# Kernel tuning notes

Measured on AMD Instinct MI355X. Metric: run time of the kernel, lower is better.

## Reference

```python
import jax, jax.numpy as jnp
import numpy as np
from jax import lax

# Model dims (match init_kwargs config)
HID = 2048      # hidden_size
NH = 64         # num_heads
P = 64          # head_dim
N = 128         # ssm_state_size
G = 1           # n_groups
CS = 256        # chunk_size
K = 4           # conv kernel
D_INNER = NH * P                  # 4096
CONV_DIM = D_INNER + 2 * G * N    # 4352
PROJ = D_INNER + CONV_DIM + NH    # 8512
EPS = 1e-5
BATCH, SEQ = 2, 2048


def setup_inputs() -> dict:
    key = jax.random.key(0)
    ks = jax.random.split(key, 8)
    hidden_states = jax.random.normal(ks[0], (BATCH, SEQ, HID), dtype=jnp.float32)
    W_in = jax.random.normal(ks[1], (PROJ, HID), dtype=jnp.float32) * 0.02
    conv_w = jax.random.normal(ks[2], (CONV_DIM, 1, K), dtype=jnp.float32) * 0.2
    conv_b = jax.random.normal(ks[3], (CONV_DIM,), dtype=jnp.float32) * 0.02
    # dt_bias initialized like inv-softplus of dt in [1e-3, 1e-1]
    dt = jnp.exp(jax.random.uniform(ks[4], (NH,)) * (np.log(0.1) - np.log(0.001)) + np.log(0.001))
    dt_bias = (dt + jnp.log(-jnp.expm1(-dt))).astype(jnp.float32)
    A_log = jnp.log(jnp.arange(1, NH + 1, dtype=jnp.float32))
    D_param = jnp.ones((NH,), dtype=jnp.float32)
    norm_w = jnp.ones((D_INNER,), dtype=jnp.float32)
    W_out = jax.random.normal(ks[5], (HID, D_INNER), dtype=jnp.float32) * 0.02
    return {"hidden_states": hidden_states, "W_in": W_in, "conv_w": conv_w,
            "conv_b": conv_b, "dt_bias": dt_bias, "A_log": A_log,
            "D_param": D_param, "norm_w": norm_w, "W_out": W_out}


def _segsum(x):
    # x: (..., c) -> (..., c, c); seg[i, j] = sum_{j < k <= i} x_k (diag 0), -inf above diag
    T = x.shape[-1]
    xc = jnp.cumsum(x, axis=-1)
    seg = xc[..., :, None] - xc[..., None, :]
    mask = jnp.tril(jnp.ones((T, T), dtype=bool))
    return jnp.where(mask, seg, -jnp.inf)


def _mamba2_forward(hidden_states, W_in, conv_w, conv_b, dt_bias, A_log, D_param, norm_w, W_out):
    B_, L_ = hidden_states.shape[:2]
    proj = hidden_states @ W_in.T                           # (b, l, PROJ)
    z = proj[..., :D_INNER]                                 # gate
    xBC = proj[..., D_INNER:D_INNER + CONV_DIM]
    dt = proj[..., D_INNER + CONV_DIM:]                     # (b, l, NH)

    # depthwise causal conv1d + silu
    xc = lax.conv_general_dilated(
        jnp.transpose(xBC, (0, 2, 1)), conv_w,
        window_strides=(1,), padding=[(K - 1, 0)],
        feature_group_count=CONV_DIM)                        # (b, CONV_DIM, l)
    xc = xc + conv_b[None, :, None]
    xBC = jax.nn.silu(jnp.transpose(xc, (0, 2, 1)))          # (b, l, CONV_DIM)

    x = xBC[..., :D_INNER].reshape(B_, L_, NH, P)
    Bm = xBC[..., D_INNER:D_INNER + G * N].reshape(B_, L_, G, N)
    Cm = xBC[..., D_INNER + G * N:].reshape(B_, L_, G, N)

    dt = jax.nn.softplus(dt + dt_bias)                       # (b, l, NH)
    A = -jnp.exp(A_log)                                      # (NH,)

    Bh = jnp.repeat(Bm, NH // G, axis=2)                     # (b, l, h, n)
    Ch = jnp.repeat(Cm, NH // G, axis=2)

    # ---- chunked SSD scan ----
    nc = L_ // CS
    x_dt = (x * dt[..., None]).reshape(B_, nc, CS, NH, P)    # (b, c, s, h, p)
    B_c = Bh.reshape(B_, nc, CS, NH, N)
    C_c = Ch.reshape(B_, nc, CS, NH, N)
    dA = jnp.transpose((dt * A).reshape(B_, nc, CS, NH), (0, 3, 1, 2))  # (b, h, c, s)
    A_cum = jnp.cumsum(dA, axis=-1)                          # (b, h, c, s)

    Lmat = jnp.exp(_segsum(dA))                              # (b, h, c, s, s)
    Y_diag = jnp.einsum('bclhn,bcshn,bhcls,bcshp->bclhp', C_c, B_c, Lmat, x_dt)

    decay_states = jnp.exp(A_cum[..., -1:] - A_cum)          # (b, h, c, s)
    states = jnp.einsum('bclhn,bhcl,bclhp->bchpn', B_c, decay_states, x_dt)

    da_last = A_cum[..., -1]                                 # (b, h, c)

    def step(prev, inp):
        s_k, d_k = inp                                       # (b,h,p,n), (b,h)
        new = prev * jnp.exp(d_k)[..., None, None] + s_k
        return new, prev

    _, prev_states = lax.scan(step, jnp.zeros((B_, NH, P, N), dtype=x.dtype),
                              (jnp.transpose(states, (1, 0, 2, 3, 4)),
                               jnp.transpose(da_last, (2, 0, 1))))
    prev_states = jnp.transpose(prev_states, (1, 2, 0, 3, 4))  # (b, h, c, p, n)

    Y_off = jnp.einsum('bclhn,bhcpn,bhcl->bclhp', C_c, prev_states, jnp.exp(A_cum))

    y = (Y_diag + Y_off).reshape(B_, L_, NH, P) + D_param[None, None, :, None] * x
    y = y.reshape(B_, L_, D_INNER)

    # gated grouped RMSNorm (norm_before_gate=False): norm(y * silu(z)) * w
    g = y * jax.nn.silu(z)
    gs = D_INNER // G
    gr = g.reshape(B_, L_, G, gs)
    var = jnp.mean(gr * gr, axis=-1, keepdims=True)
    gn = (gr * lax.rsqrt(var + EPS)).reshape(B_, L_, D_INNER) * norm_w

    return gn @ W_out.T                                      # (b, l, HID)


def reference(hidden_states, W_in, conv_w, conv_b, dt_bias, A_log, D_param, norm_w, W_out):
    return _mamba2_forward(hidden_states, W_in, conv_w, conv_b, dt_bias, A_log, D_param, norm_w, W_out)
```

## Files before the change

### kernel.cpp

```cpp
#include <hip/hip_runtime.h>

#define SEQLEN 2048
#define NHEADS 64
#define PDIM 64
#define NSTATE 128
#define CSIZE 256
#define NCHUNK 8
#define DINNER 4096
#define CONVD 4352
#define PROJD 8512

using s8v = __attribute__((ext_vector_type(8))) short;
using f4v = __attribute__((ext_vector_type(4))) float;
using bf8v = __attribute__((ext_vector_type(8))) __bf16;

__device__ __forceinline__ short f2bf(float x) {
  union { float f; unsigned u; } t; t.f = x;
  unsigned r = t.u + 0x7FFFu + ((t.u >> 16) & 1u);
  return (short)(r >> 16);
}
__device__ __forceinline__ float bf2f(short s) {
  union { unsigned u; float f; } t;
  t.u = ((unsigned)(unsigned short)s) << 16;
  return t.f;
}

__device__ __forceinline__ f4v mfma_bf16(s8v a, s8v b, f4v c) {
  return __builtin_amdgcn_mfma_f32_16x16x32_bf16(
      __builtin_bit_cast(bf8v, a), __builtin_bit_cast(bf8v, b), c, 0, 0, 0);
}

__device__ __forceinline__ void gll16(const void* g, void* l) {
  __builtin_amdgcn_global_load_lds(
      (const __attribute__((address_space(1))) unsigned*)g,
      (__attribute__((address_space(3))) unsigned*)l, 16, 0, 0);
}

__global__ __launch_bounds__(256) void cast_bf16_kernel(
    const float* __restrict__ in, short* __restrict__ out, int n4) {
  int i = blockIdx.x * 256 + threadIdx.x;
  if (i < n4) {
    float4 v = ((const float4*)in)[i];
    short4 o;
    o.x = f2bf(v.x); o.y = f2bf(v.y); o.z = f2bf(v.z); o.w = f2bf(v.w);
    ((short4*)out)[i] = o;
  }
}


#define G1_STAGE_A(dst, h, kt) do {                                          \
    _Pragma("unroll")                                                        \
    for (int it_ = 0; it_ < 2; ++it_) {                                      \
      int ci_ = it_ * 512 + tid;                                             \
      int r_ = ci_ >> 3;                                                     \
      int g_ = ((ci_ & 7) ^ (r_ & 7)) << 3;                                  \
      gll16(&A[(size_t)(tm0 + (h) * 128 + r_) * 2048 + (kt) * 64 + g_],      \
            &(dst)[(h) * 8192 + ci_ * 8]);                                   \
    }                                                                        \
  } while (0)

#define G1_STAGE_B(dst, h, kt) do {                                          \
    _Pragma("unroll")                                                        \
    for (int it_ = 0; it_ < 2; ++it_) {                                      \
      int ci_ = it_ * 512 + tid;                                             \
      int r_ = ci_ >> 3;                                                     \
      int g_ = ((ci_ & 7) ^ (r_ & 7)) << 3;                                  \
      int br_ = tn0 + (h) * 128 + r_;                                        \
      if (br_ > 8511) br_ = 8511;       \
      gll16(&B[(size_t)br_ * 2048 + (kt) * 64 + g_],                         \
            &(dst)[(h) * 8192 + ci_ * 8]);                                   \
    }                                                                        \
  } while (0)

#define RD_A(m, ks) \
  (*(const s8v*)&Ad[(wm + (m) * 16 + lr) * 64 + (((ks) * 4 + q) ^ sw7) * 8])
#define RD_B(n, ks) \
  (*(const s8v*)&Bd[(wn + (n) * 16 + lr) * 64 + (((ks) * 4 + q) ^ sw7) * 8])

#define G1_MFMA2(m0, x00, x01, x10, x11) do {                                \
    __builtin_amdgcn_s_setprio(1);                                           \
    _Pragma("unroll") for (int n = 0; n < 4; ++n)                            \
      acc[m0][n] = mfma_bf16(x00, bk0[n], acc[m0][n]);                       \
    _Pragma("unroll") for (int n = 0; n < 4; ++n)                            \
      acc[(m0) + 1][n] = mfma_bf16(x10, bk0[n], acc[(m0) + 1][n]);           \
    _Pragma("unroll") for (int n = 0; n < 4; ++n)                            \
      acc[m0][n] = mfma_bf16(x01, bk1[n], acc[m0][n]);                       \
    _Pragma("unroll") for (int n = 0; n < 4; ++n)                            \
      acc[(m0) + 1][n] = mfma_bf16(x11, bk1[n], acc[(m0) + 1][n]);           \
    __builtin_amdgcn_s_setprio(0);                                           \
  } while (0)

__global__ __launch_bounds__(512, 2) void gemm1_256(
    const short* __restrict__ A, const short* __restrict__ B,
    short* __restrict__ z, short* __restrict__ xbc, float* __restrict__ dtb,
    const float* __restrict__ dt_bias) {
  const int NT = 32;
  const int bid = blockIdx.x;
  const int sid = (bid & 7) * 68 + (bid >> 3);
  const int panel = sid / 136, rem = sid % 136;
  const int bx = rem >> 2, by = panel * 4 + (rem & 3);
  const int tm0 = by * 256, tn0 = bx * 256;
  __shared__ alignas(16) short lds[65536];
  const int tid = threadIdx.x;
  const int lane = tid & 63, wid = tid >> 6;
  const int wm = (wid >> 2) * 128, wn = (wid & 3) * 64;
  const int lr = lane & 15, q = lane >> 4;
  const int sw7 = lr & 7;

  f4v acc[8][4];
#pragma unroll
  for (int m = 0; m < 8; ++m)
#pragma unroll
    for (int n = 0; n < 4; ++n)
#pragma unroll
      for (int r = 0; r < 4; ++r) acc[m][n][r] = 0.f;

  {
    short* A0 = lds;
    short* B0 = lds + 16384;
    short* B1 = lds + 49152;
    G1_STAGE_A(A0, 0, 0); G1_STAGE_A(A0, 1, 0);
    G1_STAGE_B(B0, 0, 0); G1_STAGE_B(B0, 1, 0);
    G1_STAGE_B(B1, 0, 1); G1_STAGE_B(B1, 1, 1);
    asm volatile("s_waitcnt vmcnt(4)" ::: "memory");
    __builtin_amdgcn_s_barrier();
  }

  for (int t = 0; t < NT; ++t) {
    short* Ad = lds + ((t & 1) << 15);
    short* Bd = Ad + 16384;
    short* An = lds + (((t + 1) & 1) << 15);
    s8v bk0[4], bk1[4];
    {
#pragma unroll
      for (int n = 0; n < 4; ++n) { bk0[n] = RD_B(n, 0); bk1[n] = RD_B(n, 1); }
      s8v a00 = RD_A(0, 0), a01 = RD_A(0, 1);
      s8v a10 = RD_A(1, 0), a11 = RD_A(1, 1);
      if (t + 1 < NT) G1_STAGE_A(An, 0, t + 1);
      __builtin_amdgcn_s_barrier();
      G1_MFMA2(0, a00, a01, a10, a11);
      __builtin_amdgcn_s_barrier();
    }
    {
      s8v a00 = RD_A(2, 0), a01 = RD_A(2, 1);
      s8v a10 = RD_A(3, 0), a11 = RD_A(3, 1);
      if (t + 1 < NT) G1_STAGE_A(An, 1, t + 1);
      __builtin_amdgcn_s_barrier();
      G1_MFMA2(2, a00, a01, a10, a11);
      __builtin_amdgcn_s_barrier();
    }
    {
      s8v a00 = RD_A(4, 0), a01 = RD_A(4, 1);
      s8v a10 = RD_A(5, 0), a11 = RD_A(5, 1);
      if (t + 2 < NT) G1_STAGE_B(Bd, 0, t + 2);
      __builtin_amdgcn_s_barrier();
      G1_MFMA2(4, a00, a01, a10, a11);
      __builtin_amdgcn_s_barrier();
    }
    {
      s8v a00 = RD_A(6, 0), a01 = RD_A(6, 1);
      s8v a10 = RD_A(7, 0), a11 = RD_A(7, 1);
      if (t + 2 < NT) G1_STAGE_B(Bd, 1, t + 2);
      if (t < NT - 2) {
        asm volatile("s_waitcnt vmcnt(4)" ::: "memory");
      } else {
        asm volatile("s_waitcnt vmcnt(0)" ::: "memory");
      }
      __builtin_amdgcn_s_barrier();
      G1_MFMA2(6, a00, a01, a10, a11);
      __builtin_amdgcn_s_barrier();
    }
  }

  if (bx == 33) {
    if (wn == 0) {
#pragma unroll
      for (int m = 0; m < 8; ++m)
#pragma unroll
        for (int n = 0; n < 4; ++n) {
          int col = n * 16 + lr;
          float bias = dt_bias[col];
#pragma unroll
          for (int r = 0; r < 4; ++r) {
            int row = tm0 + wm + m * 16 + q * 4 + r;
            float v = acc[m][n][r] + bias;
            float sp = (v > 20.f) ? v : log1pf(expf(v));
            dtb[(size_t)row * NHEADS + col] = sp;
          }
        }
    }
    return;
  }
  short* outp; int stride, colbase;
  if (bx < 16) { outp = z;   stride = DINNER; colbase = tn0; }
  else         { outp = xbc; stride = CONVD;  colbase = tn0 - DINNER; }
  short* Cs = lds;
  for (int h = 0; h < 2; ++h) {
    __syncthreads();
    if ((wid >> 2) == h) {
#pragma unroll
      for (int m = 0; m < 8; ++m)
#pragma unroll
        for (int n = 0; n < 4; ++n)
#pragma unroll
          for (int r = 0; r < 4; ++r)
            Cs[(m * 16 + q * 4 + r) * 264 + wn + n * 16 + lr] =
                f2bf(acc[m][n][r]);
    }
    __syncthreads();
#pragma unroll
    for (int itr = 0; itr < 8; ++itr) {
      int idx = itr * 512 + tid;
      int r = idx >> 5, c8 = (idx & 31) * 8;
      s8v v = *(const s8v*)&Cs[r * 264 + c8];
      *(s8v*)&outp[(size_t)(tm0 + h * 128 + r) * stride + colbase + c8] = v;
    }
  }
}


#define G2_STAGE_A(dst, h, kt) do {                                          \
    _Pragma("unroll")                                                        \
    for (int it_ = 0; it_ < 2; ++it_) {                                      \
      int ci_ = it_ * 512 + tid;                                             \
      int r_ = ci_ >> 3;                                                     \
      int g_ = ((ci_ & 7) ^ (r_ & 7)) << 3;                                  \
      gll16(&Ag[(size_t)(tm0 + (h) * 128 + r_) * 4096 + (kt) * 64 + g_],     \
            &(dst)[(h) * 8192 + ci_ * 8]);                                   \
    }                                                                        \
  } while (0)

#define G2_STAGE_B(dst, h, kt) do {                                          \
    int ci_ = tid;                                                           \
    int r_ = ci_ >> 3;                                                       \
    int g_ = ((ci_ & 7) ^ (r_ & 7)) << 3;                                    \
    gll16(&Bg[(size_t)(tn0 + (h) * 64 + r_) * 4096 + (kt) * 64 + g_],        \
          &(dst)[(h) * 4096 + ci_ * 8]);                                     \
  } while (0)

#define RD_A2(m, ks) \
  (*(const s8v*)&Ad[(wm + (m) * 16 + lr) * 64 + (((ks) * 4 + q) ^ sw7) * 8])
#define RD_B2(n, ks) \
  (*(const s8v*)&Bd[(wn + (n) * 16 + lr) * 64 + (((ks) * 4 + q) ^ sw7) * 8])

#define G2_MFMA2(m0, x00, x01, x10, x11) do {                                \
    __builtin_amdgcn_s_setprio(1);                                           \
    _Pragma("unroll") for (int n = 0; n < 2; ++n)                            \
      acc[m0][n] = mfma_bf16(x00, bk0[n], acc[m0][n]);                       \
    _Pragma("unroll") for (int n = 0; n < 2; ++n)                            \
      acc[(m0) + 1][n] = mfma_bf16(x10, bk0[n], acc[(m0) + 1][n]);           \
    _Pragma("unroll") for (int n = 0; n < 2; ++n)                            \
      acc[m0][n] = mfma_bf16(x01, bk1[n], acc[m0][n]);                       \
    _Pragma("unroll") for (int n = 0; n < 2; ++n)                            \
      acc[(m0) + 1][n] = mfma_bf16(x11, bk1[n], acc[(m0) + 1][n]);           \
    __builtin_amdgcn_s_setprio(0);                                           \
  } while (0)

__global__ __launch_bounds__(512, 2) void gemm2_256x128(
    const short* __restrict__ Ag, const short* __restrict__ Bg,
    float* __restrict__ C) {
  const int NT = 64;
  const int bid = blockIdx.x;
  const int sid = (bid & 7) * 32 + (bid >> 3);
  const int panel = sid >> 6, rem = sid & 63;
  const int bx = rem >> 2, by = panel * 4 + (rem & 3);
  const int tm0 = by * 256, tn0 = bx * 128;
  __shared__ alignas(16) short lds[49152];
  const int tid = threadIdx.x;
  const int lane = tid & 63, wid = tid >> 6;
  const int wm = (wid >> 2) * 128, wn = (wid & 3) * 32;
  const int lr = lane & 15, q = lane >> 4;
  const int sw7 = lr & 7;

  f4v acc[8][2];
#pragma unroll
  for (int m = 0; m < 8; ++m)
#pragma unroll
    for (int n = 0; n < 2; ++n)
#pragma unroll
      for (int r = 0; r < 4; ++r) acc[m][n][r] = 0.f;

  {
    short* A0 = lds;
    short* B0 = lds + 16384;
    short* B1 = lds + 40960;
    G2_STAGE_A(A0, 0, 0); G2_STAGE_A(A0, 1, 0);
    G2_STAGE_B(B0, 0, 0); G2_STAGE_B(B0, 1, 0);
    G2_STAGE_B(B1, 0, 1); G2_STAGE_B(B1, 1, 1);
    asm volatile("s_waitcnt vmcnt(2)" ::: "memory");
    __builtin_amdgcn_s_barrier();
  }

  for (int t = 0; t < NT; ++t) {
    short* Ad = lds + (t & 1) * 24576;
    short* Bd = Ad + 16384;
    short* An = lds + ((t + 1) & 1) * 24576;
    s8v bk0[2], bk1[2];
    {
#pragma unroll
      for (int n = 0; n < 2; ++n) { bk0[n] = RD_B2(n, 0); bk1[n] = RD_B2(n, 1); }
      s8v a00 = RD_A2(0, 0), a01 = RD_A2(0, 1);
      s8v a10 = RD_A2(1, 0), a11 = RD_A2(1, 1);
      if (t + 1 < NT) G2_STAGE_A(An, 0, t + 1);
      __builtin_amdgcn_s_barrier();
      G2_MFMA2(0, a00, a01, a10, a11);
      __builtin_amdgcn_s_barrier();
    }
    {
      s8v a00 = RD_A2(2, 0), a01 = RD_A2(2, 1);
      s8v a10 = RD_A2(3, 0), a11 = RD_A2(3, 1);
      if (t + 1 < NT) G2_STAGE_A(An, 1, t + 1);
      __builtin_amdgcn_s_barrier();
      G2_MFMA2(2, a00, a01, a10, a11);
      __builtin_amdgcn_s_barrier();
    }
    {
      s8v a00 = RD_A2(4, 0), a01 = RD_A2(4, 1);
      s8v a10 = RD_A2(5, 0), a11 = RD_A2(5, 1);
      if (t + 2 < NT) G2_STAGE_B(Bd, 0, t + 2);
      __builtin_amdgcn_s_barrier();
      G2_MFMA2(4, a00, a01, a10, a11);
      __builtin_amdgcn_s_barrier();
    }
    {
      s8v a00 = RD_A2(6, 0), a01 = RD_A2(6, 1);
      s8v a10 = RD_A2(7, 0), a11 = RD_A2(7, 1);
      if (t + 2 < NT) G2_STAGE_B(Bd, 1, t + 2);
      if (t < NT - 2) {
        asm volatile("s_waitcnt vmcnt(2)" ::: "memory");
      } else {
        asm volatile("s_waitcnt vmcnt(0)" ::: "memory");
      }
      __builtin_amdgcn_s_barrier();
      G2_MFMA2(6, a00, a01, a10, a11);
      __builtin_amdgcn_s_barrier();
    }
  }

#pragma unroll
  for (int m = 0; m < 8; ++m)
#pragma unroll
    for (int n = 0; n < 2; ++n) {
      int r0 = tm0 + wm + m * 16 + q * 4;
      int c0 = tn0 + wn + n * 16 + lr;
#pragma unroll
      for (int r = 0; r < 4; ++r)
        C[(size_t)(r0 + r) * 2048 + c0] = acc[m][n][r];
    }
}

__global__ __launch_bounds__(256) void conv_silu_kernel(
    const short* __restrict__ xbc, const float* __restrict__ conv_w,
    const float* __restrict__ conv_b, short* __restrict__ xBCc) {
  int cc = blockIdx.x * 256 + threadIdx.x;
  int bl = blockIdx.y;
  int b = bl >> 11, l = bl & 2047;
  float4 wv = *(const float4*)&conv_w[cc * 4];
  float wk[4] = {wv.x, wv.y, wv.z, wv.w};
  float acc = conv_b[cc];
  const short* pbase = xbc + (size_t)(b * SEQLEN) * CONVD + cc;
#pragma unroll
  for (int k = 0; k < 4; k++) {
    int ls = l - 3 + k;
    if (ls >= 0) acc += bf2f(pbase[(size_t)ls * CONVD]) * wk[k];
  }
  float sv = acc / (1.f + expf(-acc));
  xBCc[(size_t)bl * CONVD + cc] = f2bf(sv);
}

__global__ __launch_bounds__(256) void ssd_states_kernel(
    const short* __restrict__ xBCc, const float* __restrict__ dtp,
    const float* __restrict__ A_log, short* __restrict__ states,
    float* __restrict__ da_last) {
  const int blk = blockIdx.x;
  const int h = blk & 63, cc = (blk >> 6) & 7, b = blk >> 9;
  const int tid = threadIdx.x;
  __shared__ float dt_s[CSIZE], Acum[CSIZE], w_s[CSIZE];
  __shared__ float xw[64][64];
  __shared__ float Bt[64][NSTATE];
  const size_t row0 = (size_t)(b * SEQLEN + cc * CSIZE);
  dt_s[tid] = dtp[(row0 + tid) * NHEADS + h];
  __syncthreads();
  if (tid == 0) {
    float Aval = -expf(A_log[h]);
    float s = 0.f;
    for (int i = 0; i < CSIZE; i++) { s += dt_s[i]; Acum[i] = s * Aval; }
    da_last[(size_t)(b * NHEADS + h) * NCHUNK + cc] = Acum[CSIZE - 1];
  }
  __syncthreads();
  float total = Acum[CSIZE - 1];
  w_s[tid] = dt_s[tid] * expf(total - Acum[tid]);
  float acc[4][8];
  for (int a = 0; a < 4; a++) for (int j = 0; j < 8; j++) acc[a][j] = 0.f;
  const int pi = (tid & 15) * 4, ni = (tid >> 4) * 8;
  for (int lt = 0; lt < 4; lt++) {
    __syncthreads();
    for (int i = 0; i < 4; i++) {
      int idx = tid + i * 256;
      int r = idx >> 4, c4 = (idx & 15) << 2;
      short4 v = *(const short4*)&xBCc[(row0 + lt * 64 + r) * CONVD + h * PDIM + c4];
      float wl = w_s[lt * 64 + r];
      xw[r][c4 + 0] = bf2f(v.x) * wl;
      xw[r][c4 + 1] = bf2f(v.y) * wl;
      xw[r][c4 + 2] = bf2f(v.z) * wl;
      xw[r][c4 + 3] = bf2f(v.w) * wl;
    }
    for (int i = 0; i < 8; i++) {
      int idx = tid + i * 256;
      int r = idx >> 5, c4 = (idx & 31) << 2;
      short4 v = *(const short4*)&xBCc[(row0 + lt * 64 + r) * CONVD + DINNER + c4];
      Bt[r][c4 + 0] = bf2f(v.x);
      Bt[r][c4 + 1] = bf2f(v.y);
      Bt[r][c4 + 2] = bf2f(v.z);
      Bt[r][c4 + 3] = bf2f(v.w);
    }
    __syncthreads();
    for (int l = 0; l < 64; l++) {
      float4 xv = *(const float4*)&xw[l][pi];
      float4 b0 = *(const float4*)&Bt[l][ni];
      float4 b1 = *(const float4*)&Bt[l][ni + 4];
      float xa[4] = {xv.x, xv.y, xv.z, xv.w};
      float bb[8] = {b0.x, b0.y, b0.z, b0.w, b1.x, b1.y, b1.z, b1.w};
      for (int a = 0; a < 4; a++)
        for (int j = 0; j < 8; j++)
          acc[a][j] += xa[a] * bb[j];
    }
  }
  const size_t sbase = (((size_t)b * NCHUNK + cc) * NHEADS + h) * (PDIM * NSTATE);
  for (int a = 0; a < 4; a++) {
    short o[8];
    for (int j = 0; j < 8; j++) o[j] = f2bf(acc[a][j]);
    *(s8v*)&states[sbase + (size_t)(pi + a) * NSTATE + ni] = *(const s8v*)o;
  }
}

__global__ __launch_bounds__(256) void scan_kernel(
    short* __restrict__ states, const float* __restrict__ da_last) {
  const int bh = blockIdx.x >> 2, sl = blockIdx.x & 3;
  const int b = bh >> 6, h = bh & 63;
  const int tid = threadIdx.x;
  float prev[8];
  for (int i = 0; i < 8; i++) prev[i] = 0.f;
  for (int c = 0; c < NCHUNK; c++) {
    const size_t base = (((size_t)b * NCHUNK + c) * NHEADS + h) * (PDIM * NSTATE)
                      + sl * 2048;
    const float d = expf(da_last[(size_t)bh * NCHUNK + c]);
    for (int i = 0; i < 8; i++) {
      size_t e = base + tid + i * 256;
      float s = bf2f(states[e]);
      states[e] = f2bf(prev[i]);
      prev[i] = prev[i] * d + s;
    }
  }
}

__global__ __launch_bounds__(256) void ssd_y_kernel(
    const short* __restrict__ xBCc, const float* __restrict__ dtp,
    const float* __restrict__ A_log, const float* __restrict__ D_param,
    const short* __restrict__ prevs, short* __restrict__ y) {
  const int blk = blockIdx.x;
  const int h = blk & 63, cc = (blk >> 6) & 7, b = blk >> 9;
  const int tid = threadIdx.x;
  const int lane = tid & 63, w = tid >> 6;
  const int lr = lane & 15, q = lane >> 4;
  __shared__ float dt_s[CSIZE];
  __shared__ float Acum[CSIZE];
  __shared__ short C_s[64][136];
  __shared__ short BP_s[64][136];
  __shared__ short xdtT[64][72];
  __shared__ short Mt[64][72];
  const size_t row0 = (size_t)(b * SEQLEN + cc * CSIZE);
  dt_s[tid] = dtp[(row0 + tid) * NHEADS + h];
  __syncthreads();
  if (tid == 0) {
    float Aval = -expf(A_log[h]);
    float s = 0.f;
    for (int i = 0; i < CSIZE; i++) { s += dt_s[i]; Acum[i] = s * Aval; }
  }
  const float Dh = D_param[h];
  const size_t prevbase = (((size_t)b * NCHUNK + cc) * NHEADS + h) * (PDIM * NSTATE);
  const int wl0 = w * 16;

  for (int lt = 0; lt < 4; lt++) {
    __syncthreads();
    for (int i = 0; i < 4; i++) {
      int idx = tid + i * 256;
      int r = idx >> 4, c8 = (idx & 15) << 3;
      *(s8v*)&C_s[r][c8] =
          *(const s8v*)&xBCc[(row0 + lt * 64 + r) * CONVD + DINNER + NSTATE + c8];
      *(s8v*)&BP_s[r][c8] = *(const s8v*)&prevs[prevbase + (size_t)r * NSTATE + c8];
    }
    __syncthreads();
    f4v acc[4];
    for (int j = 0; j < 4; j++) for (int r = 0; r < 4; r++) acc[j][r] = 0.f;
    for (int ks = 0; ks < 4; ks++) {
      s8v a = *(const s8v*)&C_s[wl0 + lr][ks * 32 + q * 8];
      for (int j = 0; j < 4; j++) {
        s8v bb = *(const s8v*)&BP_s[j * 16 + lr][ks * 32 + q * 8];
        acc[j] = mfma_bf16(a, bb, acc[j]);
      }
    }
    for (int r = 0; r < 4; r++) {
      float e = __expf(Acum[lt * 64 + wl0 + q * 4 + r]);
      for (int j = 0; j < 4; j++) acc[j][r] *= e;
    }
    for (int st = 0; st <= lt; st++) {
      __syncthreads();
      for (int i = 0; i < 4; i++) {
        int idx = tid + i * 256;
        int r = idx >> 4, c8 = (idx & 15) << 3;
        *(s8v*)&BP_s[r][c8] =
            *(const s8v*)&xBCc[(row0 + st * 64 + r) * CONVD + DINNER + c8];
      }
      for (int i = 0; i < 4; i++) {
        int idx = tid + i * 256;
        int r = idx >> 4, c4 = (idx & 15) << 2;
        float dtv = dt_s[st * 64 + r];
        short4 v = *(const short4*)&xBCc[(row0 + st * 64 + r) * CONVD + h * PDIM + c4];
        xdtT[c4 + 0][r] = f2bf(bf2f(v.x) * dtv);
        xdtT[c4 + 1][r] = f2bf(bf2f(v.y) * dtv);
        xdtT[c4 + 2][r] = f2bf(bf2f(v.z) * dtv);
        xdtT[c4 + 3][r] = f2bf(bf2f(v.w) * dtv);
      }
      __syncthreads();
      f4v sacc[4];
      for (int j = 0; j < 4; j++) for (int r = 0; r < 4; r++) sacc[j][r] = 0.f;
      for (int ks = 0; ks < 4; ks++) {
        s8v a = *(const s8v*)&C_s[wl0 + lr][ks * 32 + q * 8];
        for (int j = 0; j < 4; j++) {
          s8v bb = *(const s8v*)&BP_s[j * 16 + lr][ks * 32 + q * 8];
          sacc[j] = mfma_bf16(a, bb, sacc[j]);
        }
      }
      int lbase = lt * 64 + wl0 + q * 4;
      for (int j = 0; j < 4; j++) {
        int sg = st * 64 + j * 16 + lr;
        for (int r = 0; r < 4; r++) {
          int ll = lbase + r;
          float m = (sg <= ll) ? sacc[j][r] * __expf(Acum[ll] - Acum[sg]) : 0.f;
          Mt[wl0 + q * 4 + r][j * 16 + lr] = f2bf(m);
        }
      }
      __syncthreads();
      for (int ss2 = 0; ss2 < 2; ss2++) {
        s8v a = *(const s8v*)&Mt[wl0 + lr][ss2 * 32 + q * 8];
        for (int j = 0; j < 4; j++) {
          s8v bb = *(const s8v*)&xdtT[j * 16 + lr][ss2 * 32 + q * 8];
          acc[j] = mfma_bf16(a, bb, acc[j]);
        }
      }
    }
    for (int j = 0; j < 4; j++)
      for (int r = 0; r < 4; r++) {
        int lrow = wl0 + q * 4 + r;
        int ll = lt * 64 + lrow;
        int p = j * 16 + lr;
        float xv = bf2f(xBCc[(row0 + ll) * CONVD + h * PDIM + p]);
        Mt[lrow][p] = f2bf(acc[j][r] + Dh * xv);
      }
    __syncthreads();
    for (int ps = 0; ps < 2; ps++) {
      int r = ps * 32 + (tid >> 3);
      int c8 = (tid & 7) * 8;
      s8v v = *(const s8v*)&Mt[r][c8];
      *(s8v*)&y[(row0 + lt * 64 + r) * DINNER + h * PDIM + c8] = v;
    }
  }
}

__global__ __launch_bounds__(256) void norm_cast_kernel(
    const short* __restrict__ y, const short* __restrict__ z,
    const float* __restrict__ norm_w, short* __restrict__ g,
    const float* __restrict__ wsrc, short* __restrict__ wdst) {
  int bl = blockIdx.x, tid = threadIdx.x;
  if (bl >= 4096) {
    int base = (bl - 4096) * 1024 + tid;
#pragma unroll
    for (int i = 0; i < 4; i++) {
      int idx = base + i * 256;
      float4 v = ((const float4*)wsrc)[idx];
      short4 o;
      o.x = f2bf(v.x); o.y = f2bf(v.y); o.z = f2bf(v.z); o.w = f2bf(v.w);
      ((short4*)wdst)[idx] = o;
    }
    return;
  }
  const short4* yrow = (const short4*)(y + (size_t)bl * DINNER);
  const short4* zrow = (const short4*)(z + (size_t)bl * DINNER);
  float gv[16];
  float ss = 0.f;
  for (int i = 0; i < 4; i++) {
    short4 yv = yrow[tid + i * 256];
    short4 zv = zrow[tid + i * 256];
    float zf[4] = {bf2f(zv.x), bf2f(zv.y), bf2f(zv.z), bf2f(zv.w)};
    float yf[4] = {bf2f(yv.x), bf2f(yv.y), bf2f(yv.z), bf2f(yv.w)};
    for (int t = 0; t < 4; t++) {
      float gg = yf[t] * (zf[t] / (1.f + expf(-zf[t])));
      gv[i * 4 + t] = gg;
      ss += gg * gg;
    }
  }
  for (int off = 32; off > 0; off >>= 1) ss += __shfl_down(ss, off);
  __shared__ float red[4];
  __shared__ float rsS;
  if ((tid & 63) == 0) red[tid >> 6] = ss;
  __syncthreads();
  if (tid == 0) rsS = rsqrtf((red[0] + red[1] + red[2] + red[3]) * (1.f / 4096.f) + 1e-5f);
  __syncthreads();
  float rs = rsS;
  for (int i = 0; i < 4; i++) {
    int j4 = (tid + i * 256) * 4;
    float4 nw = *(const float4*)&norm_w[j4];
    short4 o;
    o.x = f2bf(gv[i * 4 + 0] * rs * nw.x);
    o.y = f2bf(gv[i * 4 + 1] * rs * nw.y);
    o.z = f2bf(gv[i * 4 + 2] * rs * nw.z);
    o.w = f2bf(gv[i * 4 + 3] * rs * nw.w);
    *(short4*)&g[(size_t)bl * DINNER + j4] = o;
  }
}

extern "C" void kernel_launch(void* const* d_in, const int* in_sizes, int n_in,
                              void* d_out, int out_size, void* d_ws, size_t ws_size,
                              hipStream_t stream) {
  const float* hidden  = (const float*)d_in[0];
  const float* W_in    = (const float*)d_in[1];
  const float* conv_w  = (const float*)d_in[2];
  const float* conv_b  = (const float*)d_in[3];
  const float* dt_bias = (const float*)d_in[4];
  const float* A_log   = (const float*)d_in[5];
  const float* D_param = (const float*)d_in[6];
  const float* norm_w  = (const float*)d_in[7];
  const float* W_out   = (const float*)d_in[8];
  float* out = (float*)d_out;

  char* ws = (char*)d_ws;
  short* z_bf  = (short*)(ws + 0);
  float* dtb   = (float*)(ws + 33554432);
  float* da_l  = (float*)(ws + 34603008);
  short* xbc_pre = (short*)(ws + 34607104);
  short* y_bf    = (short*)(ws + 34607104);
  short* hid_bf  = (short*)(ws + 70258688);
  short* win_bf  = (short*)(ws + 87035904);
  short* xBCc    = (short*)(ws + 70258688);
  short* states  = (short*)(ws + 105910272);
  short* g_bf    = (short*)(ws + 70258688);
  short* wout_bf = (short*)(ws + 105910272);
  if (ws_size < (size_t)122687488) return;

  cast_bf16_kernel<<<8192, 256, 0, stream>>>(hidden, hid_bf, 2097152);
  cast_bf16_kernel<<<17024, 256, 0, stream>>>(W_in, win_bf, 4358144);

  gemm1_256<<<544, 512, 0, stream>>>(hid_bf, win_bf, z_bf, xbc_pre, dtb, dt_bias);

  conv_silu_kernel<<<dim3(17, 4096), 256, 0, stream>>>(xbc_pre, conv_w, conv_b, xBCc);

  ssd_states_kernel<<<1024, 256, 0, stream>>>(xBCc, dtb, A_log, states, da_l);
  scan_kernel<<<512, 256, 0, stream>>>(states, da_l);
  ssd_y_kernel<<<1024, 256, 0, stream>>>(xBCc, dtb, A_log, D_param, states, y_bf);

  norm_cast_kernel<<<6144, 256, 0, stream>>>(y_bf, z_bf, norm_w, g_bf, W_out, wout_bf);

  gemm2_256x128<<<256, 512, 0, stream>>>(g_bf, wout_bf, out);
}
```

Baseline: 686.5 us.

## Use MFMA for chunk-state kernel and reorder GEMM MFMA issue with lgkm waits

The SSD chunk-state kernel drops its scalar FP32 outer-product loop and now stages x*w and B transposed into LDS as bf16, computing the 64x128 state with bf16 MFMA over the full 256-length chunk in one pass. Both GEMM kernels reorder MFMA issue so each accumulator row finishes its two k-slices back to back, and add an explicit lgkmcnt(0) wait before each MFMA group. The MFMA path removes most of the FP32 FMA work but rounds x*w to bf16 before accumulation, and the transposed scalar LDS stores may cause bank conflicts. The explicit waits could serialize LDS reads that the compiler would otherwise overlap with MFMAs.

```diff
diff --git a/kernel.cpp b/kernel.cpp
--- a/kernel.cpp
+++ b/kernel.cpp
@@ -82,9 +82,9 @@
     _Pragma("unroll") for (int n = 0; n < 4; ++n)                            \
       acc[m0][n] = mfma_bf16(x00, bk0[n], acc[m0][n]);                       \
     _Pragma("unroll") for (int n = 0; n < 4; ++n)                            \
+      acc[m0][n] = mfma_bf16(x01, bk1[n], acc[m0][n]);                       \
+    _Pragma("unroll") for (int n = 0; n < 4; ++n)                            \
       acc[(m0) + 1][n] = mfma_bf16(x10, bk0[n], acc[(m0) + 1][n]);           \
-    _Pragma("unroll") for (int n = 0; n < 4; ++n)                            \
-      acc[m0][n] = mfma_bf16(x01, bk1[n], acc[m0][n]);                       \
     _Pragma("unroll") for (int n = 0; n < 4; ++n)                            \
       acc[(m0) + 1][n] = mfma_bf16(x11, bk1[n], acc[(m0) + 1][n]);           \
     __builtin_amdgcn_s_setprio(0);                                           \
@@ -138,6 +138,7 @@
       s8v a10 = RD_A(1, 0), a11 = RD_A(1, 1);
       if (t + 1 < NT) G1_STAGE_A(An, 0, t + 1);
       __builtin_amdgcn_s_barrier();
+      asm volatile("s_waitcnt lgkmcnt(0)" ::: "memory");
       G1_MFMA2(0, a00, a01, a10, a11);
       __builtin_amdgcn_s_barrier();
     }
@@ -146,6 +147,7 @@
       s8v a10 = RD_A(3, 0), a11 = RD_A(3, 1);
       if (t + 1 < NT) G1_STAGE_A(An, 1, t + 1);
       __builtin_amdgcn_s_barrier();
+      asm volatile("s_waitcnt lgkmcnt(0)" ::: "memory");
       G1_MFMA2(2, a00, a01, a10, a11);
       __builtin_amdgcn_s_barrier();
     }
@@ -154,6 +156,7 @@
       s8v a10 = RD_A(5, 0), a11 = RD_A(5, 1);
       if (t + 2 < NT) G1_STAGE_B(Bd, 0, t + 2);
       __builtin_amdgcn_s_barrier();
+      asm volatile("s_waitcnt lgkmcnt(0)" ::: "memory");
       G1_MFMA2(4, a00, a01, a10, a11);
       __builtin_amdgcn_s_barrier();
     }
@@ -167,6 +170,7 @@
         asm volatile("s_waitcnt vmcnt(0)" ::: "memory");
       }
       __builtin_amdgcn_s_barrier();
+      asm volatile("s_waitcnt lgkmcnt(0)" ::: "memory");
       G1_MFMA2(6, a00, a01, a10, a11);
       __builtin_amdgcn_s_barrier();
     }
@@ -248,9 +252,9 @@
     _Pragma("unroll") for (int n = 0; n < 2; ++n)                            \
       acc[m0][n] = mfma_bf16(x00, bk0[n], acc[m0][n]);                       \
     _Pragma("unroll") for (int n = 0; n < 2; ++n)                            \
+      acc[m0][n] = mfma_bf16(x01, bk1[n], acc[m0][n]);                       \
+    _Pragma("unroll") for (int n = 0; n < 2; ++n)                            \
       acc[(m0) + 1][n] = mfma_bf16(x10, bk0[n], acc[(m0) + 1][n]);           \
-    _Pragma("unroll") for (int n = 0; n < 2; ++n)                            \
-      acc[m0][n] = mfma_bf16(x01, bk1[n], acc[m0][n]);                       \
     _Pragma("unroll") for (int n = 0; n < 2; ++n)                            \
       acc[(m0) + 1][n] = mfma_bf16(x11, bk1[n], acc[(m0) + 1][n]);           \
     __builtin_amdgcn_s_setprio(0);                                           \
@@ -303,6 +307,7 @@
       s8v a10 = RD_A2(1, 0), a11 = RD_A2(1, 1);
       if (t + 1 < NT) G2_STAGE_A(An, 0, t + 1);
       __builtin_amdgcn_s_barrier();
+      asm volatile("s_waitcnt lgkmcnt(0)" ::: "memory");
       G2_MFMA2(0, a00, a01, a10, a11);
       __builtin_amdgcn_s_barrier();
     }
@@ -311,6 +316,7 @@
       s8v a10 = RD_A2(3, 0), a11 = RD_A2(3, 1);
       if (t + 1 < NT) G2_STAGE_A(An, 1, t + 1);
       __builtin_amdgcn_s_barrier();
+      asm volatile("s_waitcnt lgkmcnt(0)" ::: "memory");
       G2_MFMA2(2, a00, a01, a10, a11);
       __builtin_amdgcn_s_barrier();
     }
@@ -319,6 +325,7 @@
       s8v a10 = RD_A2(5, 0), a11 = RD_A2(5, 1);
       if (t + 2 < NT) G2_STAGE_B(Bd, 0, t + 2);
       __builtin_amdgcn_s_barrier();
+      asm volatile("s_waitcnt lgkmcnt(0)" ::: "memory");
       G2_MFMA2(4, a00, a01, a10, a11);
       __builtin_amdgcn_s_barrier();
     }
@@ -332,6 +339,7 @@
         asm volatile("s_waitcnt vmcnt(0)" ::: "memory");
       }
       __builtin_amdgcn_s_barrier();
+      asm volatile("s_waitcnt lgkmcnt(0)" ::: "memory");
       G2_MFMA2(6, a00, a01, a10, a11);
       __builtin_amdgcn_s_barrier();
     }
@@ -375,9 +383,11 @@
   const int blk = blockIdx.x;
   const int h = blk & 63, cc = (blk >> 6) & 7, b = blk >> 9;
   const int tid = threadIdx.x;
+  const int lane = tid & 63, w = tid >> 6;
+  const int lr = lane & 15, q = lane >> 4;
   __shared__ float dt_s[CSIZE], Acum[CSIZE], w_s[CSIZE];
-  __shared__ float xw[64][64];
-  __shared__ float Bt[64][NSTATE];
+  __shared__ alignas(16) short XW[64][264];
+  __shared__ alignas(16) short BT[128][264];
   const size_t row0 = (size_t)(b * SEQLEN + cc * CSIZE);
   dt_s[tid] = dtp[(row0 + tid) * NHEADS + h];
   __syncthreads();
@@ -390,48 +400,53 @@
   __syncthreads();
   float total = Acum[CSIZE - 1];
   w_s[tid] = dt_s[tid] * expf(total - Acum[tid]);
-  float acc[4][8];
-  for (int a = 0; a < 4; a++) for (int j = 0; j < 8; j++) acc[a][j] = 0.f;
-  const int pi = (tid & 15) * 4, ni = (tid >> 4) * 8;
-  for (int lt = 0; lt < 4; lt++) {
-    __syncthreads();
+  __syncthreads();
+#pragma unroll
+  for (int lt = 0; lt < 4; ++lt) {
+#pragma unroll
     for (int i = 0; i < 4; i++) {
       int idx = tid + i * 256;
       int r = idx >> 4, c4 = (idx & 15) << 2;
       short4 v = *(const short4*)&xBCc[(row0 + lt * 64 + r) * CONVD + h * PDIM + c4];
       float wl = w_s[lt * 64 + r];
-      xw[r][c4 + 0] = bf2f(v.x) * wl;
-      xw[r][c4 + 1] = bf2f(v.y) * wl;
-      xw[r][c4 + 2] = bf2f(v.z) * wl;
-      xw[r][c4 + 3] = bf2f(v.w) * wl;
-    }
+      XW[c4 + 0][lt * 64 + r] = f2bf(bf2f(v.x) * wl);
+      XW[c4 + 1][lt * 64 + r] = f2bf(bf2f(v.y) * wl);
+      XW[c4 + 2][lt * 64 + r] = f2bf(bf2f(v.z) * wl);
+      XW[c4 + 3][lt * 64 + r] = f2bf(bf2f(v.w) * wl);
+    }
+#pragma unroll
     for (int i = 0; i < 8; i++) {
       int idx = tid + i * 256;
       int r = idx >> 5, c4 = (idx & 31) << 2;
       short4 v = *(const short4*)&xBCc[(row0 + lt * 64 + r) * CONVD + DINNER + c4];
-      Bt[r][c4 + 0] = bf2f(v.x);
-      Bt[r][c4 + 1] = bf2f(v.y);
-      Bt[r][c4 + 2] = bf2f(v.z);
-      Bt[r][c4 + 3] = bf2f(v.w);
-    }
-    __syncthreads();
-    for (int l = 0; l < 64; l++) {
-      float4 xv = *(const float4*)&xw[l][pi];
-      float4 b0 = *(const float4*)&Bt[l][ni];
-      float4 b1 = *(const float4*)&Bt[l][ni + 4];
-      float xa[4] = {xv.x, xv.y, xv.z, xv.w};
-      float bb[8] = {b0.x, b0.y, b0.z, b0.w, b1.x, b1.y, b1.z, b1.w};
-      for (int a = 0; a < 4; a++)
-        for (int j = 0; j < 8; j++)
-          acc[a][j] += xa[a] * bb[j];
+      BT[c4 + 0][lt * 64 + r] = v.x;
+      BT[c4 + 1][lt * 64 + r] = v.y;
+      BT[c4 + 2][lt * 64 + r] = v.z;
+      BT[c4 + 3][lt * 64 + r] = v.w;
+    }
+  }
+  __syncthreads();
+  f4v acc[8];
+#pragma unroll
+  for (int j = 0; j < 8; j++)
+#pragma unroll
+    for (int r = 0; r < 4; r++) acc[j][r] = 0.f;
+#pragma unroll
+  for (int kc = 0; kc < 8; ++kc) {
+    s8v a = *(const s8v*)&XW[w * 16 + lr][kc * 32 + q * 8];
+#pragma unroll
+    for (int j = 0; j < 8; ++j) {
+      s8v bb = *(const s8v*)&BT[j * 16 + lr][kc * 32 + q * 8];
+      acc[j] = mfma_bf16(a, bb, acc[j]);
     }
   }
   const size_t sbase = (((size_t)b * NCHUNK + cc) * NHEADS + h) * (PDIM * NSTATE);
-  for (int a = 0; a < 4; a++) {
-    short o[8];
-    for (int j = 0; j < 8; j++) o[j] = f2bf(acc[a][j]);
-    *(s8v*)&states[sbase + (size_t)(pi + a) * NSTATE + ni] = *(const s8v*)o;
-  }
+#pragma unroll
+  for (int j = 0; j < 8; ++j)
+#pragma unroll
+    for (int r = 0; r < 4; ++r)
+      states[sbase + (size_t)(w * 16 + q * 4 + r) * NSTATE + j * 16 + lr] =
+          f2bf(acc[j][r]);
 }
 
 __global__ __launch_bounds__(256) void scan_kernel(
```

Result: no change. 699.3 us (+1.9%).
